# Performance work log

Measured on AMD Instinct MI355X. Metric: run time of the kernel, lower is better.

Reference implementation:

```python
import jax, jax.numpy as jnp
import numpy as np

N = 50000; E = 800000; NFEAT = 128; NHID = 64; CONCAT = 2; NCLASS = 40
D = CONCAT * NHID
BN_EPS = 1e-5


def setup_inputs() -> dict:
    key = jax.random.key(0)
    ks = jax.random.split(key, 16)
    rn = lambda k, s, sc=0.05: jax.random.normal(k, s, jnp.float32) * sc
    return {
        "x1a": rn(ks[0], (N, NFEAT), 1.0),
        "x1b": rn(ks[1], (N, NFEAT), 1.0),
        "x2a": rn(ks[2], (N, NFEAT), 1.0),
        "x2b": rn(ks[3], (N, NFEAT), 1.0),
        "edge_index1": jax.random.randint(ks[4], (2, E), 0, N),
        "edge_index2": jax.random.randint(ks[5], (2, E), 0, N),
        "Wi": rn(ks[6], (CONCAT, NFEAT, NHID)),
        "bi": jnp.zeros((CONCAT, NHID), jnp.float32),
        "gi": jnp.ones((CONCAT, NHID), jnp.float32),
        "bei": jnp.zeros((CONCAT, NHID), jnp.float32),
        "Wm": rn(ks[7], (2, D, D)),
        "bm": jnp.zeros((2, D), jnp.float32),
        "gm": jnp.ones((2, D), jnp.float32),
        "bem": jnp.zeros((2, D), jnp.float32),
        "Wf": rn(ks[8], (D, NCLASS)),
        "bf": jnp.zeros((NCLASS,), jnp.float32),
        "fc1w1_W": rn(ks[9], (D,)),
        "fc1w1_b": jnp.zeros((1,), jnp.float32),
        "fc1w2_W": rn(ks[10], (D,)),
        "fc1w2_b": jnp.zeros((1,), jnp.float32),
        "aws_w1_W": rn(ks[11], (2, D)),
        "aws_w1_b": jnp.zeros((2,), jnp.float32),
        "aws_w2_W": rn(ks[12], (2, D)),
        "aws_w2_b": jnp.zeros((2,), jnp.float32),
        "fcw1_W": rn(ks[13], (NCLASS,)),
        "fcw1_b": jnp.zeros((1,), jnp.float32),
        "fcw2_W": rn(ks[14], (NCLASS,)),
        "fcw2_b": jnp.zeros((1,), jnp.float32),
    }


def _gcn_norm(edge_index, n):
    # GCN symmetric normalization with self-loops (cached=True behaviour)
    loop = jnp.arange(n)
    src = jnp.concatenate([edge_index[0], loop])
    dst = jnp.concatenate([edge_index[1], loop])
    deg = jax.ops.segment_sum(jnp.ones_like(dst, jnp.float32), dst, n)
    dinv = jnp.where(deg > 0, deg ** -0.5, 0.0)
    return src, dst, dinv[src] * dinv[dst]


def _gcn(x, W, b, g):
    # GCNConv: dense projection then sparse scatter-based aggregation
    src, dst, norm = g
    h = x @ W
    agg = jax.ops.segment_sum(h[src] * norm[:, None], dst, x.shape[0])
    return agg + b


def _bn(x, gamma, beta):
    m = x.mean(0)
    v = jnp.mean((x - m) ** 2, axis=0)
    return (x - m) * jax.lax.rsqrt(v + BN_EPS) * gamma + beta


def _gate(x1, x2, w1, b1, w2, b2):
    # sigmoid gates L1-normalized; only the last node's row is used (w[-1,:])
    s1 = jax.nn.sigmoid(jnp.dot(x1[-1], w1) + b1)
    s2 = jax.nn.sigmoid(jnp.dot(x2[-1], w2) + b2)
    t = s1 + s2
    return s1 / t, s2 / t


def _forward(x1a, x1b, x2a, x2b, g1, g2, Wi, bi, gi, bei, Wm, bm, gm, bem,
             Wf, bf, fc1w1_W, fc1w1_b, fc1w2_W, fc1w2_b,
             aws_w1_W, aws_w1_b, aws_w2_W, aws_w2_b,
             fcw1_W, fcw1_b, fcw2_W, fcw2_b):
    xs1, xs2 = (x1a, x1b), (x2a, x2b)
    h1 = jnp.concatenate([jax.nn.relu(_bn(_gcn(xs1[i], Wi[i], bi[i], g1), gi[i], bei[i]))
                          for i in range(CONCAT)], axis=-1)
    h2 = jnp.concatenate([jax.nn.relu(_bn(_gcn(xs2[i], Wi[i], bi[i], g2), gi[i], bei[i]))
                          for i in range(CONCAT)], axis=-1)
    w1, w2 = _gate(h1, h2, fc1w1_W, fc1w1_b[0], fc1w2_W, fc1w2_b[0])
    x = w1 * h1 + w2 * h2
    for i in range(Wm.shape[0]):  # middle layers (n_layers - 2)
        a = jax.nn.relu(_bn(_gcn(x, Wm[i], bm[i], g1), gm[i], bem[i]))
        b = jax.nn.relu(_bn(_gcn(x, Wm[i], bm[i], g2), gm[i], bem[i]))
        w1, w2 = _gate(a, b, aws_w1_W[i], aws_w1_b[i], aws_w2_W[i], aws_w2_b[i])
        x = w1 * a + w2 * b
    p1 = _gcn(x, Wf, bf, g1)
    p2 = _gcn(x, Wf, bf, g2)
    w1, w2 = _gate(p1, p2, fcw1_W, fcw1_b[0], fcw2_W, fcw2_b[0])
    return (w1 * p1 + w2 * p2, p1, p2)


def reference(x1a, x1b, x2a, x2b, edge_index1, edge_index2, Wi, bi, gi, bei,
              Wm, bm, gm, bem, Wf, bf, fc1w1_W, fc1w1_b, fc1w2_W, fc1w2_b,
              aws_w1_W, aws_w1_b, aws_w2_W, aws_w2_b,
              fcw1_W, fcw1_b, fcw2_W, fcw2_b):
    g1 = _gcn_norm(edge_index1, N)
    g2 = _gcn_norm(edge_index2, N)
    return _forward(x1a, x1b, x2a, x2b, g1, g2, Wi, bi, gi, bei, Wm, bm, gm, bem,
                    Wf, bf, fc1w1_W, fc1w1_b, fc1w2_W, fc1w2_b,
                    aws_w1_W, aws_w1_b, aws_w2_W, aws_w2_b,
                    fcw1_W, fcw1_b, fcw2_W, fcw2_b)
```

## Files before the change

kernel.cpp:

```cpp
#include <hip/hip_runtime.h>
#include <hip/hip_fp16.h>


#define DFEAT 128

typedef __attribute__((ext_vector_type(8))) short bf16x8;
typedef __attribute__((ext_vector_type(4))) float f32x4;

__device__ __forceinline__ unsigned short f2bf(float f) {
    unsigned u = __float_as_uint(f);
    u += 0x7fffu + ((u >> 16) & 1u);
    return (unsigned short)(u >> 16);
}
__device__ __forceinline__ float bf2f(unsigned short u) {
    return __uint_as_float((unsigned)u << 16);
}
__device__ __forceinline__ unsigned f2h16(float f) {
    return (unsigned)__half_as_ushort(__float2half(f));
}
__device__ __forceinline__ float h16f(unsigned u) {
    return __half2float(__ushort_as_half((unsigned short)u));
}
__device__ __forceinline__ float4 bf4tof4(ushort4 u) {
    return make_float4(__uint_as_float((unsigned)u.x << 16),
// ... 40 lines not shown
        int s = src[i];
        buf[i - e0] = (d << 16) | s;
        atomicAdd(&cnt8[d >> RSH], 1);
    }
    __syncthreads();
    if (t == 0) {
        int run = 0;
        for (int r = 0; r < nr; ++r) { pre8[r] = run; run += cnt8[r]; }
        pre8[nr] = run;
    }
    __syncthreads();
    if (t < nr) {
        base8[t] = atomicAdd(&gcount[g * NRMAX + t], cnt8[t]);
        cnt8[t] = 0;
    }
    __syncthreads();
    for (int j = t; j < ec; j += 256) {
        int v = buf[j];
        int d = (unsigned)v >> 16;
        int r = d >> RSH;
        int p = pre8[r] + atomicAdd(&cnt8[r], 1);
        buf2[p] = ((d & (RSZ - 1)) << 16) | (v & 0xFFFF);
    }
    __syncthreads();
    for (int j = t; j < ec; j += 256) {
        int r = 0;
        while (j >= pre8[r + 1]) ++r;
        int gpos = base8[r] + (j - pre8[r]);
        if (gpos < SCAP) stg[((size_t)g * NRMAX + r) * SCAP + gpos] = buf2[j];
    }
}

__global__ __launch_bounds__(256) void histB_kernel(
    const int* __restrict__ stg, const int* __restrict__ gcount,
    int* __restrict__ baseB, int nr) {
    int g = blockIdx.y;
    int r = blockIdx.x / SUBS;
    int sub = blockIdx.x % SUBS;
    __shared__ int hist[RSZ];
    int t = threadIdx.x;
    for (int i = t; i < RSZ; i += 256) hist[i] = 0;
    __syncthreads();
    int len = min(gcount[g * NRMAX + r], SCAP);
    int seg = (len + SUBS - 1) / SUBS;
    int e0 = sub * seg, e1 = min(e0 + seg, len);
    const int* sp = stg + ((size_t)g * NRMAX + r) * SCAP;
    for (int i = e0 + t; i < e1; i += 256) atomicAdd(&hist[(unsigned)sp[i] >> 16], 1);
    __syncthreads();
    int* bp = baseB + (((size_t)(g * NRMAX + r) * SUBS + sub) << RSH);
    for (int i = t; i < RSZ; i += 256) bp[i] = hist[i];
}

__global__ __launch_bounds__(256) void scanB_kernel(
    int* __restrict__ baseB, int* __restrict__ cnt1, int* __restrict__ cnt2, int n) {
    int node = blockIdx.x * 256 + threadIdx.x;
    int g = blockIdx.y;
    if (node >= n) return;
    int r = node >> RSH, dloc = node & (RSZ - 1);
    int* p = baseB + (((size_t)(g * NRMAX + r) * SUBS) << RSH) + dloc;
    int run = 0;
#pragma unroll
    for (int s = 0; s < SUBS; ++s) {
        int v = p[(size_t)s << RSH];
        p[(size_t)s << RSH] = run;
        run += v;
    }
    (g ? cnt2 : cnt1)[node] = run;
}

__global__ __launch_bounds__(256) void fillC_kernel(
    const int* __restrict__ stg, const int* __restrict__ gcount,
    const int* __restrict__ baseB,
    const int* __restrict__ rp1, const int* __restrict__ rp2,
    const float* __restrict__ dv1, const float* __restrict__ dv2,
    int* __restrict__ cs1, int* __restrict__ cs2, int n, int nr) {
    int g = blockIdx.y;
    int r = blockIdx.x / SUBS;
    int sub = blockIdx.x % SUBS;
    const int* rp = g ? rp2 : rp1;
    const float* dv = g ? dv2 : dv1;
    int* cs = g ? cs2 : cs1;
    __shared__ int off[RSZ];
    int t = threadIdx.x;
    int r0 = r << RSH;
    int rn = min(RSZ, n - r0);
    if (rn <= 0) return;
    const int* bp = baseB + (((size_t)(g * NRMAX + r) * SUBS + sub) << RSH);
    for (int i = t; i < rn; i += 256) off[i] = bp[i] + rp[r0 + i];
    __syncthreads();
    int len = min(gcount[g * NRMAX + r], SCAP);
    int seg = (len + SUBS - 1) / SUBS;
    int e0 = sub * seg, e1 = min(e0 + seg, len);
    const int* sp = stg + ((size_t)g * NRMAX + r) * SCAP;
    for (int i = e0 + t; i < e1; i += 256) {
        int v = sp[i];
        int dloc = (unsigned)v >> 16;
        int s = v & 0xFFFF;
        float w = dv[r0 + dloc] * dv[s];
        int pos = atomicAdd(&off[dloc], 1);
        cs[pos] = (int)((f2h16(w) << 16) | (unsigned)s);
    }
}

__global__ __launch_bounds__(256) void blocksum_kernel(const int* __restrict__ c1,
                                                       const int* __restrict__ c2,
                                                       int* __restrict__ bs, int n, int nb) {
    const int* c = blockIdx.y ? c2 : c1;
    int* out = bs + (size_t)blockIdx.y * nb;
    int t = threadIdx.x;
    int base = blockIdx.x * 2048 + t * 8;
    int s = 0;
#pragma unroll
    for (int i = 0; i < 8; ++i) {
        int idx = base + i;
        if (idx < n) s += c[idx];
    }
    __shared__ int red[256];
    red[t] = s;
    __syncthreads();
    for (int o = 128; o > 0; o >>= 1) {
        if (t < o) red[t] += red[t + o];
        __syncthreads();
    }
    if (t == 0) out[blockIdx.x] = red[0];
}

__global__ void scansums_kernel(int* __restrict__ bs, int nb, int* __restrict__ rp1,
                                int* __restrict__ rp2, int n, int E, float* __restrict__ stats) {
    int t = threadIdx.x;
    if (t < 2) {
        int* b = bs + (size_t)t * nb;
        int run = 0;
        for (int i = 0; i < nb; ++i) {
            int v = b[i];
            b[i] = run;
            run += v;
        }
        (t ? rp2 : rp1)[n] = E;
    }
    for (int i = t; i < 512; i += 64) stats[i] = 0.f;
}

__global__ __launch_bounds__(256) void writerp_kernel(const int* __restrict__ c1,
                                                      const int* __restrict__ c2,
                                                      const int* __restrict__ bs,
                                                      int* __restrict__ rp1, int* __restrict__ rp2,
                                                      float* __restrict__ dv1,
                                                      float* __restrict__ dv2, int n, int nb) {
    const int* c = blockIdx.y ? c2 : c1;
    int* rp = blockIdx.y ? rp2 : rp1;
    float* dv = blockIdx.y ? dv2 : dv1;
    int boff = bs[(size_t)blockIdx.y * nb + blockIdx.x];
    int t = threadIdx.x;
    int base = blockIdx.x * 2048 + t * 8;
    int v[8];
    int s = 0;
#pragma unroll
    for (int i = 0; i < 8; ++i) {
        int idx = base + i;
        v[i] = (idx < n) ? c[idx] : 0;
        s += v[i];
    }
    __shared__ int red[256];
    red[t] = s;
    __syncthreads();
    for (int o = 1; o < 256; o <<= 1) {
        int x = (t >= o) ? red[t - o] : 0;
        __syncthreads();
        red[t] += x;
        __syncthreads();
    }
    int run = boff + red[t] - s;
#pragma unroll
    for (int i = 0; i < 8; ++i) {
        int idx = base + i;
        if (idx < n) {
            rp[idx] = run;
            dv[idx] = rsqrtf((float)(v[i] + 1));
            run += v[i];
        }
    }
}

template <int COLS, typename OutT>
__global__ __launch_bounds__(256) void dualagg_kernel(
    const unsigned short* __restrict__ h1, const unsigned short* __restrict__ h2,
    const int* __restrict__ rp1, const int* __restrict__ cs1, const float* __restrict__ dv1,
    const int* __restrict__ rp2, const int* __restrict__ cs2, const float* __restrict__ dv2,
    const float* __restrict__ bias, OutT* __restrict__ o1, OutT* __restrict__ o2, int n) {
    constexpr int ACT = COLS / 8;
    const unsigned short* h;
    const int *rp, *cs;
    const float* dv;
    OutT* out;
    if (blockIdx.y == 0) { h = h1; rp = rp1; cs = cs1; dv = dv1; out = o1; }
    else                 { h = h2; rp = rp2; cs = cs2; dv = dv2; out = o2; }
    int wid = blockIdx.x * 4 + (threadIdx.x >> 6);
    if (wid >= n) return;
    int lane = threadIdx.x & 63;
    int grp = lane >> 4;
    int li = lane & 15;
    bool act = li < ACT;
    float acc[8] = {0.f, 0.f, 0.f, 0.f, 0.f, 0.f, 0.f, 0.f};
    int e0 = rp[wid], e1 = rp[wid + 1];
    int e = e0 + grp;
    for (; e + 4 < e1; e += 8) {
        int va = cs[e], vb = cs[e + 4];
        float wa = h16f((unsigned)va >> 16); int sa = va & 0xFFFF;
        float wb = h16f((unsigned)vb >> 16); int sb = vb & 0xFFFF;
        if (act) {
            int4 ra = *(const int4*)(h + (size_t)sa * COLS + li * 8);
            int4 rb = *(const int4*)(h + (size_t)sb * COLS + li * 8);
            acc8(acc, wa, ra);
            acc8(acc, wb, rb);
        }
    }
    if (e < e1) {
        int va = cs[e];
        float wa = h16f((unsigned)va >> 16); int sa = va & 0xFFFF;
        if (act) {
            int4 ra = *(const int4*)(h + (size_t)sa * COLS + li * 8);
            acc8(acc, wa, ra);
        }
    }
#pragma unroll
    for (int j = 0; j < 8; ++j) {
        acc[j] += __shfl_xor(acc[j], 16);
        acc[j] += __shfl_xor(acc[j], 32);
    }
    if (grp == 0 && act) {
        float dn = dv[wid];
        float w = dn * dn;
        int4 rs = *(const int4*)(h + (size_t)wid * COLS + li * 8);
        acc8(acc, w, rs);
        float4 b0 = ((const float4*)bias)[li * 2];
        float4 b1 = ((const float4*)bias)[li * 2 + 1];
        acc[0] += b0.x; acc[1] += b0.y; acc[2] += b0.z; acc[3] += b0.w;
        acc[4] += b1.x; acc[5] += b1.y; acc[6] += b1.z; acc[7] += b1.w;
        if constexpr (sizeof(OutT) == 4) {
            float* op = (float*)out + (size_t)wid * COLS + li * 8;
            *(float4*)op = make_float4(acc[0], acc[1], acc[2], acc[3]);
            *(float4*)(op + 4) = make_float4(acc[4], acc[5], acc[6], acc[7]);
        } else {
            int4 o;
            o.x = (int)((unsigned)f2bf(acc[0]) | ((unsigned)f2bf(acc[1]) << 16));
            o.y = (int)((unsigned)f2bf(acc[2]) | ((unsigned)f2bf(acc[3]) << 16));
            o.z = (int)((unsigned)f2bf(acc[4]) | ((unsigned)f2bf(acc[5]) << 16));
            o.w = (int)((unsigned)f2bf(acc[6]) | ((unsigned)f2bf(acc[7]) << 16));
            *(int4*)((unsigned short*)out + (size_t)wid * COLS + li * 8) = o;
        }
    }
}

__global__ __launch_bounds__(256) void prepW1_kernel(const float* __restrict__ Wi,
                                                     unsigned short* __restrict__ Wt1) {
    int o = blockIdx.x * 256 + threadIdx.x;
    int kk = o & 31;
    int col = (o >> 5) & 63;
    int kc = (o >> 11) & 3;
    int h = (o >> 13) & 1;
    int s = (o >> 14) & 1;
    float w = Wi[(size_t)s * 8192 + (size_t)(kc * 32 + kk) * 64 + col];
    unsigned short hi = f2bf(w);
    Wt1[o] = h ? f2bf(w - bf2f(hi)) : hi;
}

__global__ __launch_bounds__(256) void gemm_l1_kernel(
    const float* __restrict__ x1a, const float* __restrict__ x1b, const float* __restrict__ x2a,
    const float* __restrict__ x2b, const unsigned short* __restrict__ Wt1,
    unsigned short* __restrict__ H1, unsigned short* __restrict__ H2, int nrows) {
    const float* X = (blockIdx.y == 0) ? x1a : (blockIdx.y == 1) ? x1b
                     : (blockIdx.y == 2) ? x2a : x2b;
    int slice = blockIdx.y & 1;
    unsigned short* Y = (blockIdx.y < 2) ? H1 : H2;
    int ocol = slice * 64;
    int tid = threadIdx.x;
    int row0 = blockIdx.x * 64;
    int wave = tid >> 6, lane = tid & 63;
    int m = lane & 15, quad = lane >> 4;
    int arow = row0 + wave * 16 + m;
    bool rv = arow < nrows;
    const float* xp = X + (size_t)arow * DFEAT;
    const unsigned short* Whp = Wt1 + (size_t)slice * 16384;
    const unsigned short* Wlp = Whp + 8192;
    f32x4 acc[4];
#pragma unroll
    for (int i = 0; i < 4; ++i) acc[i] = (f32x4){0.f, 0.f, 0.f, 0.f};
#pragma unroll
    for (int kc = 0; kc < 4; ++kc) {
        float4 f0 = make_float4(0.f, 0.f, 0.f, 0.f);
        float4 f1 = make_float4(0.f, 0.f, 0.f, 0.f);
        if (rv) {
            f0 = *(const float4*)(xp + kc * 32 + quad * 8);
            f1 = *(const float4*)(xp + kc * 32 + quad * 8 + 4);
        }
        float fs[8] = {f0.x, f0.y, f0.z, f0.w, f1.x, f1.y, f1.z, f1.w};
        bf16x8 ah, al;
#pragma unroll
        for (int j = 0; j < 8; ++j) {
            unsigned short hh = f2bf(fs[j]);
            ah[j] = (short)hh;
            al[j] = (short)f2bf(fs[j] - bf2f(hh));
        }
#pragma unroll
        for (int ct = 0; ct < 4; ++ct) {
            int wo = kc * 2048 + (ct * 16 + m) * 32 + quad * 8;
            bf16x8 bh = *(const bf16x8*)(Whp + wo);
            bf16x8 bl = *(const bf16x8*)(Wlp + wo);
            acc[ct] = __builtin_amdgcn_mfma_f32_16x16x32_bf16(ah, bh, acc[ct], 0, 0, 0);
            acc[ct] = __builtin_amdgcn_mfma_f32_16x16x32_bf16(al, bh, acc[ct], 0, 0, 0);
            acc[ct] = __builtin_amdgcn_mfma_f32_16x16x32_bf16(ah, bl, acc[ct], 0, 0, 0);
        }
    }
#pragma unroll
    for (int ct = 0; ct < 4; ++ct) {
#pragma unroll
        for (int i = 0; i < 4; ++i) {
            int gr = row0 + wave * 16 + quad * 4 + i;
            if (gr < nrows) Y[(size_t)gr * DFEAT + ocol + ct * 16 + m] = f2bf(acc[ct][i]);
        }
    }
}

__global__ __launch_bounds__(256) void prepW_kernel(const float* __restrict__ Wm,
                                                    unsigned short* __restrict__ Wt) {
    int o = blockIdx.x * 256 + threadIdx.x;
    int l = blockIdx.y;
    int kk = o & 31;
    int col = (o >> 5) & 127;
    int kc = o >> 12;
    int k = kc * 32 + kk;
    Wt[(size_t)l * 16384 + o] = f2bf(Wm[(size_t)l * 16384 + (size_t)k * 128 + col]);
}

__global__ __launch_bounds__(256) void gemm_mfma_kernel(
    const unsigned short* __restrict__ Abf, const unsigned short* __restrict__ Bbf,
    const float* __restrict__ ss, const float* __restrict__ wout,
    const unsigned short* __restrict__ Wt, unsigned short* __restrict__ Y, int nrows) {
    __shared__ unsigned short Xs[64 * 128];
    int tid = threadIdx.x;
    int row0 = blockIdx.x * 64;
    int wave = tid >> 6, lane = tid & 63;
    int m = lane & 15, quad = lane >> 4;
    float w1 = wout[0], w2 = wout[1];
    for (int u = tid; u < 1024; u += 256) {
        int r = u >> 4;
        int col0 = (u & 15) * 8;
        int gr = row0 + r;
        int swz = (r & 7) << 3;
        if (gr < nrows) {
#pragma unroll
            for (int hh = 0; hh < 2; ++hh) {
                int c = col0 + hh * 4;
                float4 fa = bf4tof4(*(const ushort4*)(Abf + (size_t)gr * 128 + c));
                float4 fb = bf4tof4(*(const ushort4*)(Bbf + (size_t)gr * 128 + c));
                float4 sa = *(const float4*)(ss + c);
                float4 ha = *(const float4*)(ss + 128 + c);
                float4 sb = *(const float4*)(ss + 256 + c);
                float4 hb = *(const float4*)(ss + 384 + c);
                ushort4 o;
                o.x = f2bf(w1 * fmaxf(fmaf(fa.x, sa.x, ha.x), 0.f) +
                           w2 * fmaxf(fmaf(fb.x, sb.x, hb.x), 0.f));
                o.y = f2bf(w1 * fmaxf(fmaf(fa.y, sa.y, ha.y), 0.f) +
                           w2 * fmaxf(fmaf(fb.y, sb.y, hb.y), 0.f));
                o.z = f2bf(w1 * fmaxf(fmaf(fa.z, sa.z, ha.z), 0.f) +
                           w2 * fmaxf(fmaf(fb.z, sb.z, hb.z), 0.f));
                o.w = f2bf(w1 * fmaxf(fmaf(fa.w, sa.w, ha.w), 0.f) +
                           w2 * fmaxf(fmaf(fb.w, sb.w, hb.w), 0.f));
                *(ushort4*)&Xs[r * 128 + (c ^ swz)] = o;
            }
        } else {
            ushort4 z = {0, 0, 0, 0};
            *(ushort4*)&Xs[r * 128 + (col0 ^ swz)] = z;
            *(ushort4*)&Xs[r * 128 + ((col0 + 4) ^ swz)] = z;
        }
    }
    __syncthreads();
    f32x4 acc[8];
#pragma unroll
    for (int i = 0; i < 8; ++i) acc[i] = (f32x4){0.f, 0.f, 0.f, 0.f};
    int arow = wave * 16 + m;
#pragma unroll
    for (int kc = 0; kc < 4; ++kc) {
        int ac = (kc * 32 + quad * 8) ^ ((arow & 7) << 3);
        bf16x8 a = *(const bf16x8*)&Xs[arow * 128 + ac];
// ... 49 lines not shown
            int gr = row0 + r;
            int col0 = kc * 32 + c * 4;
            float4 v = make_float4(0.f, 0.f, 0.f, 0.f);
            if (gr < nrows) {
                float4 a = bf4tof4(*(const ushort4*)(Abf + (size_t)gr * DFEAT + col0));
                float4 b = bf4tof4(*(const ushort4*)(Bbf + (size_t)gr * DFEAT + col0));
                float4 scA = *(const float4*)(ss + col0);
                float4 shA = *(const float4*)(ss + DFEAT + col0);
                float4 scB = *(const float4*)(ss + 2 * DFEAT + col0);
                float4 shB = *(const float4*)(ss + 3 * DFEAT + col0);
                v.x = w1 * fmaxf(fmaf(a.x, scA.x, shA.x), 0.f) +
                      w2 * fmaxf(fmaf(b.x, scB.x, shB.x), 0.f);
                v.y = w1 * fmaxf(fmaf(a.y, scA.y, shA.y), 0.f) +
                      w2 * fmaxf(fmaf(b.y, scB.y, shB.y), 0.f);
                v.z = w1 * fmaxf(fmaf(a.z, scA.z, shA.z), 0.f) +
                      w2 * fmaxf(fmaf(b.z, scB.z, shB.z), 0.f);
                v.w = w1 * fmaxf(fmaf(a.w, scA.w, shA.w), 0.f) +
                      w2 * fmaxf(fmaf(b.w, scB.w, shB.w), 0.f);
            }
            Xs[r][c * 4 + 0] = v.x;
            Xs[r][c * 4 + 1] = v.y;
            Xs[r][c * 4 + 2] = v.z;
            Xs[r][c * 4 + 3] = v.w;
        }
        __syncthreads();
#pragma unroll
        for (int k = 0; k < 32; ++k) {
            float4 w = *(float4*)&Ws[k][cg * 4];
#pragma unroll
            for (int i = 0; i < RPT; ++i) {
                float a = Xs[rg * RPT + i][k];
                acc[i].x = fmaf(a, w.x, acc[i].x);
                acc[i].y = fmaf(a, w.y, acc[i].y);
                acc[i].z = fmaf(a, w.z, acc[i].z);
                acc[i].w = fmaf(a, w.w, acc[i].w);
            }
        }
        __syncthreads();
    }
    if (cg * 4 < fout) {
#pragma unroll
        for (int i = 0; i < RPT; ++i) {
            int r = row0 + rg * RPT + i;
            if (r < nrows) {
                ushort4 o;
                o.x = f2bf(acc[i].x); o.y = f2bf(acc[i].y);
                o.z = f2bf(acc[i].z); o.w = f2bf(acc[i].w);
                *(ushort4*)(Y + (size_t)r * ostride + cg * 4) = o;
            }
        }
    }
}

__global__ __launch_bounds__(256) void stats2_kernel(const unsigned short* __restrict__ A,
                                                     const unsigned short* __restrict__ B,
                                                     float* __restrict__ stats, int nrows) {
    __shared__ float red1[256];
    __shared__ float red2[256];
    int t = threadIdx.x;
    int col = t & 127;
    int rg = t >> 7;
    const unsigned short* src = (blockIdx.y == 0) ? A : B;
    float* st = stats + (size_t)blockIdx.y * 256;
    int r0 = blockIdx.x * 128 + rg * 64;
    int r1 = min(r0 + 64, nrows);
    float s = 0.f, s2 = 0.f;
    for (int r = r0; r < r1; ++r) {
        float v = bf2f(src[(size_t)r * DFEAT + col]);
        s += v;
        s2 = fmaf(v, v, s2);
    }
    red1[t] = s;
    red2[t] = s2;
    __syncthreads();
    if (t < 128) {
        atomicAdd(&st[col], red1[t] + red1[t + 128]);
        atomicAdd(&st[DFEAT + col], red2[t] + red2[t + 128]);
    }
}

__global__ __launch_bounds__(128) void gate_prep_kernel(
    float* __restrict__ statsA, float* __restrict__ statsB,
    const unsigned short* __restrict__ preA, const unsigned short* __restrict__ preB,
    const float* __restrict__ gamma, const float* __restrict__ beta,
    const float* __restrict__ gwA, const float* __restrict__ gbA,
    const float* __restrict__ gwB, const float* __restrict__ gbB,
    float* __restrict__ ss, float* __restrict__ wout, int nrows) {
    __shared__ float red[128];
    __shared__ float dotA_s;
    int t = threadIdx.x;
    float invN = 1.f / (float)nrows;
    float meanA = statsA[t] * invN;
    float varA = statsA[DFEAT + t] * invN - meanA * meanA;
    float scA = gamma[t] * rsqrtf(varA + 1e-5f);
    float shA = beta[t] - meanA * scA;
    ss[t] = scA;
    ss[DFEAT + t] = shA;
    float meanB = statsB[t] * invN;
    float varB = statsB[DFEAT + t] * invN - meanB * meanB;
    float scB = gamma[t] * rsqrtf(varB + 1e-5f);
    float shB = beta[t] - meanB * scB;
    ss[2 * DFEAT + t] = scB;
    ss[3 * DFEAT + t] = shB;
    statsA[t] = 0.f;
    statsA[DFEAT + t] = 0.f;
    statsB[t] = 0.f;
    statsB[DFEAT + t] = 0.f;
    float av = fmaxf(fmaf(bf2f(preA[(size_t)(nrows - 1) * DFEAT + t]), scA, shA), 0.f);
    red[t] = av * gwA[t];
    __syncthreads();
    for (int s = 64; s > 0; s >>= 1) {
        if (t < s) red[t] += red[t + s];
        __syncthreads();
    }
    if (t == 0) dotA_s = red[0];
    __syncthreads();
    float bv = fmaxf(fmaf(bf2f(preB[(size_t)(nrows - 1) * DFEAT + t]), scB, shB), 0.f);
    red[t] = bv * gwB[t];
    __syncthreads();
    for (int s = 64; s > 0; s >>= 1) {
        if (t < s) red[t] += red[t + s];
        __syncthreads();
    }
    if (t == 0) {
        float s1 = 1.f / (1.f + expf(-(dotA_s + gbA[0])));
        float s2 = 1.f / (1.f + expf(-(red[0] + gbB[0])));
        float tt = s1 + s2;
        wout[0] = s1 / tt;
        wout[1] = s2 / tt;
    }
}

__global__ __launch_bounds__(64) void gate_final_kernel(
    const float* __restrict__ p1, const float* __restrict__ p2,
    const float* __restrict__ w1v, const float* __restrict__ b1,
    const float* __restrict__ w2v, const float* __restrict__ b2,
    float* __restrict__ wout, int nrows, int nclass) {
    __shared__ float red[64];
    __shared__ float dot1_s;
    int t = threadIdx.x;
    float v = (t < nclass) ? p1[(size_t)(nrows - 1) * nclass + t] * w1v[t] : 0.f;
    red[t] = v;
    __syncthreads();
    for (int s = 32; s > 0; s >>= 1) {
        if (t < s) red[t] += red[t + s];
        __syncthreads();
    }
    if (t == 0) dot1_s = red[0];
    __syncthreads();
    v = (t < nclass) ? p2[(size_t)(nrows - 1) * nclass + t] * w2v[t] : 0.f;
    red[t] = v;
    __syncthreads();
    for (int s = 32; s > 0; s >>= 1) {
        if (t < s) red[t] += red[t + s];
        __syncthreads();
    }
    if (t == 0) {
        float s1 = 1.f / (1.f + expf(-(dot1_s + b1[0])));
        float s2 = 1.f / (1.f + expf(-(red[0] + b2[0])));
        float tt = s1 + s2;
        wout[0] = s1 / tt;
        wout[1] = s2 / tt;
    }
}

__global__ __launch_bounds__(256) void mix_kernel(const float* __restrict__ p1,
                                                  const float* __restrict__ p2,
                                                  const float* __restrict__ wout,
                                                  float* __restrict__ o, int n4) {
    int idx = blockIdx.x * blockDim.x + threadIdx.x;
    if (idx >= n4) return;
// ... 12 lines not shown
    const int E = in_sizes[4] / 2;
    const int NC = in_sizes[15];

    const float* x1a = (const float*)d_in[0];
    const float* x1b = (const float*)d_in[1];
    const float* x2a = (const float*)d_in[2];
    const float* x2b = (const float*)d_in[3];
    const int* ei1 = (const int*)d_in[4];
    const int* ei2 = (const int*)d_in[5];
    const float* Wi = (const float*)d_in[6];
    const float* bi = (const float*)d_in[7];
    const float* gi = (const float*)d_in[8];
    const float* bei = (const float*)d_in[9];
    const float* Wm = (const float*)d_in[10];
    const float* bm = (const float*)d_in[11];
    const float* gm = (const float*)d_in[12];
    const float* bem = (const float*)d_in[13];
    const float* Wf = (const float*)d_in[14];
    const float* bf = (const float*)d_in[15];
    const float* fc1w1_W = (const float*)d_in[16];
    const float* fc1w1_b = (const float*)d_in[17];
    const float* fc1w2_W = (const float*)d_in[18];
    const float* fc1w2_b = (const float*)d_in[19];
    const float* aws_w1_W = (const float*)d_in[20];
    const float* aws_w1_b = (const float*)d_in[21];
    const float* aws_w2_W = (const float*)d_in[22];
    const float* aws_w2_b = (const float*)d_in[23];
    const float* fcw1_W = (const float*)d_in[24];
    const float* fcw1_b = (const float*)d_in[25];
    const float* fcw2_W = (const float*)d_in[26];
    const float* fcw2_b = (const float*)d_in[27];

    char* ws = (char*)d_ws;
    size_t off = 0;
    auto alloc = [&](size_t bytes) -> char* {
        char* p = ws + off;
        off += (bytes + 255) & ~(size_t)255;
        return p;
    };
    unsigned short* A = (unsigned short*)alloc((size_t)N * DFEAT * 2);
    unsigned short* B = (unsigned short*)alloc((size_t)N * DFEAT * 2);
    unsigned short* H1 = (unsigned short*)alloc((size_t)N * DFEAT * 2);
    unsigned short* H2 = (unsigned short*)alloc((size_t)N * DFEAT * 2);
    int* rp1 = (int*)alloc((size_t)(N + 1) * 4);
    int* rp2 = (int*)alloc((size_t)(N + 1) * 4);
    int* cnt1 = (int*)alloc((size_t)N * 4);
    int* cnt2 = (int*)alloc((size_t)N * 4);
    float* dv1 = (float*)alloc((size_t)N * 4);
    float* dv2 = (float*)alloc((size_t)N * 4);
    int* cs1 = (int*)alloc((size_t)E * 4);
    int* cs2 = (int*)alloc((size_t)E * 4);
    int* stg = (int*)alloc((size_t)2 * NRMAX * SCAP * 4);
    int* baseB = (int*)alloc(((size_t)2 * NRMAX * SUBS << RSH) * 4);
    int* gcount = (int*)alloc(2 * NRMAX * 4);
    unsigned short* Wt = (unsigned short*)alloc((size_t)2 * 16384 * 2);
    unsigned short* Wt1 = (unsigned short*)alloc((size_t)32768 * 2);
    float* stats = (float*)alloc(2048);
    float* statsA = stats;
    float* statsB = stats + 256;
    float* ssbuf = (float*)alloc(2048);
    float* wout = (float*)alloc(256);
    int nb = (N + 2047) / 2048;
    int* bsums = (int*)alloc((size_t)2 * nb * 4);

    const int* src1 = ei1;
    const int* dst1 = ei1 + E;
    const int* src2 = ei2;
    const int* dst2 = ei2 + E;

    int nr = (N + RSZ - 1) >> RSH;
    int gemmbl = (N + 63) / 64;
    dim3 pagrid((E + EPA - 1) / EPA, 2);
    dim3 rsgrid(nr * SUBS, 2);
    dim3 ssgrid((N + 255) / 256, 2);
    dim3 agggrid((N + 3) / 4, 2);
    dim3 statgrid((N + 127) / 128, 2);
    dim3 scangrid(nb, 2);
    dim3 l1grid(gemmbl, 4);
    dim3 prepgrid(64, 2);

    hipMemsetAsync(gcount, 0, 2 * NRMAX * 4, stream);
    prepW_kernel<<<prepgrid, 256, 0, stream>>>(Wm, Wt);
    prepW1_kernel<<<128, 256, 0, stream>>>(Wi, Wt1);
    partA_kernel<<<pagrid, 256, 0, stream>>>(src1, dst1, src2, dst2, stg, gcount, E, nr);
    histB_kernel<<<rsgrid, 256, 0, stream>>>(stg, gcount, baseB, nr);
    scanB_kernel<<<ssgrid, 256, 0, stream>>>(baseB, cnt1, cnt2, N);
    blocksum_kernel<<<scangrid, 256, 0, stream>>>(cnt1, cnt2, bsums, N, nb);
    scansums_kernel<<<1, 64, 0, stream>>>(bsums, nb, rp1, rp2, N, E, stats);
    writerp_kernel<<<scangrid, 256, 0, stream>>>(cnt1, cnt2, bsums, rp1, rp2, dv1, dv2, N, nb);
    fillC_kernel<<<rsgrid, 256, 0, stream>>>(stg, gcount, baseB, rp1, rp2, dv1, dv2,
                                             cs1, cs2, N, nr);

    gemm_l1_kernel<<<l1grid, 256, 0, stream>>>(x1a, x1b, x2a, x2b, Wt1, H1, H2, N);
    dualagg_kernel<128, unsigned short><<<agggrid, 256, 0, stream>>>(
        H1, H2, rp1, cs1, dv1, rp2, cs2, dv2, bi, A, B, N);
    stats2_kernel<<<statgrid, 256, 0, stream>>>(A, B, stats, N);
    gate_prep_kernel<<<1, 128, 0, stream>>>(statsA, statsB, A, B, gi, bei, fc1w1_W, fc1w1_b,
                                            fc1w2_W, fc1w2_b, ssbuf, wout, N);

    gemm_mfma_kernel<<<gemmbl, 256, 0, stream>>>(A, B, ssbuf, wout, Wt, H1, N);
    dualagg_kernel<128, unsigned short><<<agggrid, 256, 0, stream>>>(
        H1, H1, rp1, cs1, dv1, rp2, cs2, dv2, bm, A, B, N);
    stats2_kernel<<<statgrid, 256, 0, stream>>>(A, B, stats, N);
    gate_prep_kernel<<<1, 128, 0, stream>>>(statsA, statsB, A, B, gm, bem, aws_w1_W, aws_w1_b,
                                            aws_w2_W, aws_w2_b, ssbuf, wout, N);

    gemm_mfma_kernel<<<gemmbl, 256, 0, stream>>>(A, B, ssbuf, wout, Wt + 16384, H1, N);
    dualagg_kernel<128, unsigned short><<<agggrid, 256, 0, stream>>>(
        H1, H1, rp1, cs1, dv1, rp2, cs2, dv2, bm + 128, A, B, N);
    stats2_kernel<<<statgrid, 256, 0, stream>>>(A, B, stats, N);
    gate_prep_kernel<<<1, 128, 0, stream>>>(statsA, statsB, A, B, gm + 128, bem + 128,
                                            aws_w1_W + 128, aws_w1_b + 1, aws_w2_W + 128,
                                            aws_w2_b + 1, ssbuf, wout, N);

    float* out0 = (float*)d_out;
    float* p1 = out0 + (size_t)N * NC;
    float* p2 = out0 + (size_t)2 * N * NC;
    gemm_fused_kernel<16, 4><<<gemmbl, 256, 0, stream>>>(A, B, ssbuf, wout, Wf, H2, N, NC, NC);
    dualagg_kernel<40, float><<<agggrid, 256, 0, stream>>>(H2, H2, rp1, cs1, dv1, rp2, cs2, dv2,
                                                           bf, p1, p2, N);
    gate_final_kernel<<<1, 64, 0, stream>>>(p1, p2, fcw1_W, fcw1_b, fcw2_W, fcw2_b, wout, N, NC);
    mix_kernel<<<(N * NC / 4 + 255) / 256, 256, 0, stream>>>(p1, p2, wout, out0, N * NC / 4);
}
```

Baseline: 668.6 us.

## Split 128-col aggregation by column halves and fuse small prep/scan/gate kernels

The 128-wide aggregation kernel is now split across two column halves (grid z), with 8 lanes per edge group and 8 edge groups per wave. The goal is more parallelism and 16 edges in flight per wave. Several small kernels are merged: the two weight-prep kernels and the memset become one prep kernel, the block sums move into scanB, and the BN/gate prep runs in the last block of the stats kernel through an atomic ticket. The gather work per edge is duplicated across the two column halves, and the last-block pattern relies on fences and atomic reads.

Result: slower. 861.5 us (+28.8%).

```diff
diff --git a/kernel.cpp b/kernel.cpp
--- a/kernel.cpp
+++ b/kernel.cpp
@@ -116,20 +116,73 @@
 }
 
 __global__ __launch_bounds__(256) void scanB_kernel(
-    int* __restrict__ baseB, int* __restrict__ cnt1, int* __restrict__ cnt2, int n) {
+    int* __restrict__ baseB, int* __restrict__ cnt1, int* __restrict__ cnt2,
+    int* __restrict__ bsums, int n, int nb) {
     int node = blockIdx.x * 256 + threadIdx.x;
     int g = blockIdx.y;
-    if (node >= n) return;
-    int r = node >> RSH, dloc = node & (RSZ - 1);
-    int* p = baseB + (((size_t)(g * NRMAX + r) * SUBS) << RSH) + dloc;
+    int t = threadIdx.x;
     int run = 0;
-#pragma unroll
-    for (int s = 0; s < SUBS; ++s) {
-        int v = p[(size_t)s << RSH];
-        p[(size_t)s << RSH] = run;
-        run += v;
-    }
-    (g ? cnt2 : cnt1)[node] = run;
+    if (node < n) {
+        int r = node >> RSH, dloc = node & (RSZ - 1);
+        int* p = baseB + (((size_t)(g * NRMAX + r) * SUBS) << RSH) + dloc;
+#pragma unroll
+        for (int s = 0; s < SUBS; ++s) {
+            int v = p[(size_t)s << RSH];
+            p[(size_t)s << RSH] = run;
+            run += v;
+        }
+        (g ? cnt2 : cnt1)[node] = run;
+    }
+    __shared__ int red[256];
+    red[t] = run;
+    __syncthreads();
+    for (int o = 128; o > 0; o >>= 1) {
+        if (t < o) red[t] += red[t + o];
+        __syncthreads();
+    }
+    if (t == 0) bsums[(size_t)g * nb + blockIdx.x] = red[0];
+}
+
+__global__ void scansums_kernel(int* __restrict__ bs, int nb, int* __restrict__ rp1,
+                                int* __restrict__ rp2, int n, int E, float* __restrict__ stats) {
+    int t = threadIdx.x;
+    if (t < 2) {
+        int* b = bs + (size_t)t * nb;
+        int run = 0;
+        for (int i = 0; i < nb; ++i) {
+            int v = b[i];
+            b[i] = run;
+            run += v;
+        }
+        (t ? rp2 : rp1)[n] = E;
+    }
+    for (int i = t; i < 512; i += 64) stats[i] = 0.f;
+}
+
+__global__ __launch_bounds__(256) void writerp_kernel(
+    const int* __restrict__ c1, const int* __restrict__ c2, const int* __restrict__ bs,
+    int* __restrict__ rp1, int* __restrict__ rp2,
+    float* __restrict__ dv1, float* __restrict__ dv2, int n, int nb) {
+    const int* c = blockIdx.y ? c2 : c1;
+    int* rp = blockIdx.y ? rp2 : rp1;
+    float* dv = blockIdx.y ? dv2 : dv1;
+    int t = threadIdx.x;
+    int node = blockIdx.x * 256 + t;
+    int v = (node < n) ? c[node] : 0;
+    __shared__ int red[256];
+    red[t] = v;
+    __syncthreads();
+    for (int o = 1; o < 256; o <<= 1) {
+        int x = (t >= o) ? red[t - o] : 0;
+        __syncthreads();
+        red[t] += x;
+        __syncthreads();
+    }
+    if (node < n) {
+        int run = bs[(size_t)blockIdx.y * nb + blockIdx.x] + red[t] - v;
+        rp[node] = run;
+        dv[node] = rsqrtf((float)(v + 1));
+    }
 }
 
 __global__ __launch_bounds__(256) void fillC_kernel(
@@ -166,97 +219,77 @@
     }
 }
 
-__global__ __launch_bounds__(256) void blocksum_kernel(const int* __restrict__ c1,
-                                                       const int* __restrict__ c2,
-                                                       int* __restrict__ bs, int n, int nb) {
-    const int* c = blockIdx.y ? c2 : c1;
-    int* out = bs + (size_t)blockIdx.y * nb;
-    int t = threadIdx.x;
-    int base = blockIdx.x * 2048 + t * 8;
-    int s = 0;
-#pragma unroll
-    for (int i = 0; i < 8; ++i) {
-        int idx = base + i;
-        if (idx < n) s += c[idx];
-    }
-    __shared__ int red[256];
-    red[t] = s;
-    __syncthreads();
-    for (int o = 128; o > 0; o >>= 1) {
-        if (t < o) red[t] += red[t + o];
-        __syncthreads();
-    }
-    if (t == 0) out[blockIdx.x] = red[0];
-}
-
-__global__ void scansums_kernel(int* __restrict__ bs, int nb, int* __restrict__ rp1,
-                                int* __restrict__ rp2, int n, int E, float* __restrict__ stats) {
-    int t = threadIdx.x;
-    if (t < 2) {
-        int* b = bs + (size_t)t * nb;
-        int run = 0;
-        for (int i = 0; i < nb; ++i) {
-            int v = b[i];
-            b[i] = run;
-            run += v;
-        }
-        (t ? rp2 : rp1)[n] = E;
-    }
-    for (int i = t; i < 512; i += 64) stats[i] = 0.f;
-}
-
-__global__ __launch_bounds__(256) void writerp_kernel(const int* __restrict__ c1,
-                                                      const int* __restrict__ c2,
-                                                      const int* __restrict__ bs,
-                                                      int* __restrict__ rp1, int* __restrict__ rp2,
-                                                      float* __restrict__ dv1,
-                                                      float* __restrict__ dv2, int n, int nb) {
-    const int* c = blockIdx.y ? c2 : c1;
-    int* rp = blockIdx.y ? rp2 : rp1;
-    float* dv = blockIdx.y ? dv2 : dv1;
-    int boff = bs[(size_t)blockIdx.y * nb + blockIdx.x];
-    int t = threadIdx.x;
-    int base = blockIdx.x * 2048 + t * 8;
-    int v[8];
-    int s = 0;
-#pragma unroll
-    for (int i = 0; i < 8; ++i) {
-        int idx = base + i;
-        v[i] = (idx < n) ? c[idx] : 0;
-        s += v[i];
-    }
-    __shared__ int red[256];
-    red[t] = s;
-    __syncthreads();
-    for (int o = 1; o < 256; o <<= 1) {
-        int x = (t >= o) ? red[t - o] : 0;
-        __syncthreads();
-        red[t] += x;
-        __syncthreads();
-    }
-    int run = boff + red[t] - s;
-#pragma unroll
-    for (int i = 0; i < 8; ++i) {
-        int idx = base + i;
-        if (idx < n) {
-            rp[idx] = run;
-            dv[idx] = rsqrtf((float)(v[i] + 1));
-            run += v[i];
-        }
-    }
-}
-
-template <int COLS, typename OutT>
-__global__ __launch_bounds__(256) void dualagg_kernel(
+__global__ __launch_bounds__(256) void dualagg128_kernel(
     const unsigned short* __restrict__ h1, const unsigned short* __restrict__ h2,
     const int* __restrict__ rp1, const int* __restrict__ cs1, const float* __restrict__ dv1,
     const int* __restrict__ rp2, const int* __restrict__ cs2, const float* __restrict__ dv2,
-    const float* __restrict__ bias, OutT* __restrict__ o1, OutT* __restrict__ o2, int n) {
+    const float* __restrict__ bias, unsigned short* __restrict__ o1,
+    unsigned short* __restrict__ o2, int n) {
+    const unsigned short* h;
+    const int *rp, *cs;
+    const float* dv;
+    unsigned short* out;
+    if (blockIdx.y == 0) { h = h1; rp = rp1; cs = cs1; dv = dv1; out = o1; }
+    else                 { h = h2; rp = rp2; cs = cs2; dv = dv2; out = o2; }
+    int wid = blockIdx.x * 4 + (threadIdx.x >> 6);
+    if (wid >= n) return;
+    int lane = threadIdx.x & 63;
+    int grp = lane >> 3;
+    int li = lane & 7;
+    int colbase = (int)blockIdx.z * 64 + li * 8;
+    float acc[8] = {0.f, 0.f, 0.f, 0.f, 0.f, 0.f, 0.f, 0.f};
+    int e0 = rp[wid], e1 = rp[wid + 1];
+    int e = e0 + grp;
+    for (; e + 8 < e1; e += 16) {
+        int va = cs[e], vb = cs[e + 8];
+        float wa = h16f((unsigned)va >> 16); int sa = va & 0xFFFF;
+        float wb = h16f((unsigned)vb >> 16); int sb = vb & 0xFFFF;
+        int4 ra = *(const int4*)(h + (size_t)sa * 128 + colbase);
+        int4 rb = *(const int4*)(h + (size_t)sb * 128 + colbase);
+        acc8(acc, wa, ra);
+        acc8(acc, wb, rb);
+    }
+    if (e < e1) {
+        int va = cs[e];
+        float wa = h16f((unsigned)va >> 16); int sa = va & 0xFFFF;
+        int4 ra = *(const int4*)(h + (size_t)sa * 128 + colbase);
+        acc8(acc, wa, ra);
+    }
+#pragma unroll
+    for (int j = 0; j < 8; ++j) {
+        acc[j] += __shfl_xor(acc[j], 8);
+        acc[j] += __shfl_xor(acc[j], 16);
+        acc[j] += __shfl_xor(acc[j], 32);
+    }
+    if (grp == 0) {
+        float dn = dv[wid];
+        float w = dn * dn;
+        int4 rs = *(const int4*)(h + (size_t)wid * 128 + colbase);
+        acc8(acc, w, rs);
+        float4 b0 = *(const float4*)(bias + colbase);
+        float4 b1 = *(const float4*)(bias + colbase + 4);
+        acc[0] += b0.x; acc[1] += b0.y; acc[2] += b0.z; acc[3] += b0.w;
+        acc[4] += b1.x; acc[5] += b1.y; acc[6] += b1.z; acc[7] += b1.w;
+        int4 o;
+        o.x = (int)((unsigned)f2bf(acc[0]) | ((unsigned)f2bf(acc[1]) << 16));
+        o.y = (int)((unsigned)f2bf(acc[2]) | ((unsigned)f2bf(acc[3]) << 16));
+        o.z = (int)((unsigned)f2bf(acc[4]) | ((unsigned)f2bf(acc[5]) << 16));
+        o.w = (int)((unsigned)f2bf(acc[6]) | ((unsigned)f2bf(acc[7]) << 16));
+        *(int4*)(out + (size_t)wid * 128 + colbase) = o;
+    }
+}
+
+__global__ __launch_bounds__(256) void dualagg_final_kernel(
+    const unsigned short* __restrict__ h1, const unsigned short* __restrict__ h2,
+    const int* __restrict__ rp1, const int* __restrict__ cs1, const float* __restrict__ dv1,
+    const int* __restrict__ rp2, const int* __restrict__ cs2, const float* __restrict__ dv2,
+    const float* __restrict__ bias, float* __restrict__ o1, float* __restrict__ o2, int n) {
+    constexpr int COLS = 40;
     constexpr int ACT = COLS / 8;
     const unsigned short* h;
     const int *rp, *cs;
     const float* dv;
-    OutT* out;
+    float* out;
     if (blockIdx.y == 0) { h = h1; rp = rp1; cs = cs1; dv = dv1; out = o1; }
     else                 { h = h2; rp = rp2; cs = cs2; dv = dv2; out = o2; }
     int wid = blockIdx.x * 4 + (threadIdx.x >> 6);
@@ -301,32 +334,40 @@
         float4 b1 = ((const float4*)bias)[li * 2 + 1];
         acc[0] += b0.x; acc[1] += b0.y; acc[2] += b0.z; acc[3] += b0.w;
         acc[4] += b1.x; acc[5] += b1.y; acc[6] += b1.z; acc[7] += b1.w;
-        if constexpr (sizeof(OutT) == 4) {
-            float* op = (float*)out + (size_t)wid * COLS + li * 8;
-            *(float4*)op = make_float4(acc[0], acc[1], acc[2], acc[3]);
-            *(float4*)(op + 4) = make_float4(acc[4], acc[5], acc[6], acc[7]);
-        } else {
-            int4 o;
-            o.x = (int)((unsigned)f2bf(acc[0]) | ((unsigned)f2bf(acc[1]) << 16));
-            o.y = (int)((unsigned)f2bf(acc[2]) | ((unsigned)f2bf(acc[3]) << 16));
-            o.z = (int)((unsigned)f2bf(acc[4]) | ((unsigned)f2bf(acc[5]) << 16));
-            o.w = (int)((unsigned)f2bf(acc[6]) | ((unsigned)f2bf(acc[7]) << 16));
-            *(int4*)((unsigned short*)out + (size_t)wid * COLS + li * 8) = o;
-        }
-    }
-}
-
-__global__ __launch_bounds__(256) void prepW1_kernel(const float* __restrict__ Wi,
-                                                     unsigned short* __restrict__ Wt1) {
-    int o = blockIdx.x * 256 + threadIdx.x;
-    int kk = o & 31;
-    int col = (o >> 5) & 63;
-    int kc = (o >> 11) & 3;
-    int h = (o >> 13) & 1;
-    int s = (o >> 14) & 1;
-    float w = Wi[(size_t)s * 8192 + (size_t)(kc * 32 + kk) * 64 + col];
-    unsigned short hi = f2bf(w);
-    Wt1[o] = h ? f2bf(w - bf2f(hi)) : hi;
+        float* op = out + (size_t)wid * COLS + li * 8;
+        *(float4*)op = make_float4(acc[0], acc[1], acc[2], acc[3]);
+        *(float4*)(op + 4) = make_float4(acc[4], acc[5], acc[6], acc[7]);
+    }
+}
+
+__global__ __launch_bounds__(256) void prep_kernel(const float* __restrict__ Wm,
+                                                   const float* __restrict__ Wi,
+                                                   unsigned short* __restrict__ Wt,
+                                                   unsigned short* __restrict__ Wt1,
+                                                   int* __restrict__ zeros) {
+    int b = blockIdx.x;
+    int t = threadIdx.x;
+    if (b < 128) {
+        int l = b >> 6;
+        int o = (b & 63) * 256 + t;
+        int kk = o & 31;
+        int col = (o >> 5) & 127;
+        int kc = o >> 12;
+        int k = kc * 32 + kk;
+        Wt[(size_t)l * 16384 + o] = f2bf(Wm[(size_t)l * 16384 + (size_t)k * 128 + col]);
+    } else if (b < 256) {
+        int o = (b - 128) * 256 + t;
+        int kk = o & 31;
+        int col = (o >> 5) & 63;
+        int kc = (o >> 11) & 3;
+        int hsel = (o >> 13) & 1;
+        int s = (o >> 14) & 1;
+        float w = Wi[(size_t)s * 8192 + (size_t)(kc * 32 + kk) * 64 + col];
+        unsigned short hi = f2bf(w);
+        Wt1[o] = hsel ? f2bf(w - bf2f(hi)) : hi;
+    } else {
+        if (t < 32) zeros[t] = 0;
+    }
 }
 
 __global__ __launch_bounds__(256) void gemm_l1_kernel(
@@ -384,17 +425,6 @@
             if (gr < nrows) Y[(size_t)gr * DFEAT + ocol + ct * 16 + m] = f2bf(acc[ct][i]);
         }
     }
-}
-
-__global__ __launch_bounds__(256) void prepW_kernel(const float* __restrict__ Wm,
-                                                    unsigned short* __restrict__ Wt) {
-    int o = blockIdx.x * 256 + threadIdx.x;
-    int l = blockIdx.y;
-    int kk = o & 31;
-    int col = (o >> 5) & 127;
-    int kc = o >> 12;
-    int k = kc * 32 + kk;
-    Wt[(size_t)l * 16384 + o] = f2bf(Wm[(size_t)l * 16384 + (size_t)k * 128 + col]);
 }
 
 __global__ __launch_bounds__(256) void gemm_mfma_kernel(
@@ -550,62 +580,74 @@
     }
 }
 
-__global__ __launch_bounds__(256) void stats2_kernel(const unsigned short* __restrict__ A,
-                                                     const unsigned short* __restrict__ B,
-                                                     float* __restrict__ stats, int nrows) {
+__global__ __launch_bounds__(256) void stats2g_kernel(
+    const unsigned short* __restrict__ A, const unsigned short* __restrict__ B,
+    float* __restrict__ stats, int nrows,
+    const float* __restrict__ gamma, const float* __restrict__ beta,
+    const float* __restrict__ gwA, const float* __restrict__ gbA,
+    const float* __restrict__ gwB, const float* __restrict__ gbB,
+    float* __restrict__ ss, float* __restrict__ wout, unsigned* __restrict__ tick) {
     __shared__ float red1[256];
     __shared__ float red2[256];
     int t = threadIdx.x;
-    int col = t & 127;
-    int rg = t >> 7;
-    const unsigned short* src = (blockIdx.y == 0) ? A : B;
-    float* st = stats + (size_t)blockIdx.y * 256;
-    int r0 = blockIdx.x * 128 + rg * 64;
-    int r1 = min(r0 + 64, nrows);
-    float s = 0.f, s2 = 0.f;
-    for (int r = r0; r < r1; ++r) {
-        float v = bf2f(src[(size_t)r * DFEAT + col]);
-        s += v;
-        s2 = fmaf(v, v, s2);
-    }
-    red1[t] = s;
-    red2[t] = s2;
-    __syncthreads();
-    if (t < 128) {
-        atomicAdd(&st[col], red1[t] + red1[t + 128]);
-        atomicAdd(&st[DFEAT + col], red2[t] + red2[t + 128]);
-    }
-}
-
-__global__ __launch_bounds__(128) void gate_prep_kernel(
-    float* __restrict__ statsA, float* __restrict__ statsB,
-    const unsigned short* __restrict__ preA, const unsigned short* __restrict__ preB,
-    const float* __restrict__ gamma, const float* __restrict__ beta,
-    const float* __restrict__ gwA, const float* __restrict__ gbA,
-    const float* __restrict__ gwB, const float* __restrict__ gbB,
-    float* __restrict__ ss, float* __restrict__ wout, int nrows) {
+    {
+        int col = t & 127;
+        int rg = t >> 7;
+        const unsigned short* src = (blockIdx.y == 0) ? A : B;
+        float* st = stats + (size_t)blockIdx.y * 256;
+        int r0 = blockIdx.x * 128 + rg * 64;
+        int r1 = min(r0 + 64, nrows);
+        float s = 0.f, s2 = 0.f;
+        for (int r = r0; r < r1; ++r) {
+            float v = bf2f(src[(size_t)r * DFEAT + col]);
+            s += v;
+            s2 = fmaf(v, v, s2);
+        }
+        red1[t] = s;
+        red2[t] = s2;
+        __syncthreads();
+        if (t < 128) {
+            atomicAdd(&st[col], red1[t] + red1[t + 128]);
+            atomicAdd(&st[DFEAT + col], red2[t] + red2[t + 128]);
+        }
+    }
+    __threadfence();
+    __shared__ int amlast;
+    __syncthreads();
+    if (t == 0) {
+        unsigned v = atomicAdd(tick, 1u);
+        amlast = (v == gridDim.x * gridDim.y - 1) ? 1 : 0;
+    }
+    __syncthreads();
+    if (!amlast) return;
     __shared__ float red[128];
     __shared__ float dotA_s;
-    int t = threadIdx.x;
     float invN = 1.f / (float)nrows;
-    float meanA = statsA[t] * invN;
-    float varA = statsA[DFEAT + t] * invN - meanA * meanA;
-    float scA = gamma[t] * rsqrtf(varA + 1e-5f);
-    float shA = beta[t] - meanA * scA;
-    ss[t] = scA;
-    ss[DFEAT + t] = shA;
-    float meanB = statsB[t] * invN;
-    float varB = statsB[DFEAT + t] * invN - meanB * meanB;
-    float scB = gamma[t] * rsqrtf(varB + 1e-5f);
-    float shB = beta[t] - meanB * scB;
-    ss[2 * DFEAT + t] = scB;
-    ss[3 * DFEAT + t] = shB;
-    statsA[t] = 0.f;
-    statsA[DFEAT + t] = 0.f;
-    statsB[t] = 0.f;
-    statsB[DFEAT + t] = 0.f;
-    float av = fmaxf(fmaf(bf2f(preA[(size_t)(nrows - 1) * DFEAT + t]), scA, shA), 0.f);
-    red[t] = av * gwA[t];
+    float scA = 0.f, shA = 0.f, scB = 0.f, shB = 0.f;
+    if (t < 128) {
+        float sA = atomicAdd(&stats[t], 0.f);
+        float s2A = atomicAdd(&stats[DFEAT + t], 0.f);
+        float sB = atomicAdd(&stats[256 + t], 0.f);
+        float s2B = atomicAdd(&stats[256 + DFEAT + t], 0.f);
+        float meanA = sA * invN;
+        float varA = s2A * invN - meanA * meanA;
+        scA = gamma[t] * rsqrtf(varA + 1e-5f);
+        shA = beta[t] - meanA * scA;
+        ss[t] = scA;
+        ss[DFEAT + t] = shA;
+        float meanB = sB * invN;
+        float varB = s2B * invN - meanB * meanB;
+        scB = gamma[t] * rsqrtf(varB + 1e-5f);
+        shB = beta[t] - meanB * scB;
+        ss[2 * DFEAT + t] = scB;
+        ss[3 * DFEAT + t] = shB;
+        stats[t] = 0.f;
+        stats[DFEAT + t] = 0.f;
+        stats[256 + t] = 0.f;
+        stats[256 + DFEAT + t] = 0.f;
+        float av = fmaxf(fmaf(bf2f(A[(size_t)(nrows - 1) * DFEAT + t]), scA, shA), 0.f);
+        red[t] = av * gwA[t];
+    }
     __syncthreads();
     for (int s = 64; s > 0; s >>= 1) {
         if (t < s) red[t] += red[t + s];
@@ -613,8 +655,10 @@
     }
     if (t == 0) dotA_s = red[0];
     __syncthreads();
-    float bv = fmaxf(fmaf(bf2f(preB[(size_t)(nrows - 1) * DFEAT + t]), scB, shB), 0.f);
-    red[t] = bv * gwB[t];
+    if (t < 128) {
+        float bv = fmaxf(fmaf(bf2f(B[(size_t)(nrows - 1) * DFEAT + t]), scB, shB), 0.f);
+        red[t] = bv * gwB[t];
+    }
     __syncthreads();
     for (int s = 64; s > 0; s >>= 1) {
         if (t < s) red[t] += red[t + s];
@@ -733,15 +777,14 @@
     int* cs2 = (int*)alloc((size_t)E * 4);
     int* stg = (int*)alloc((size_t)2 * NRMAX * SCAP * 4);
     int* baseB = (int*)alloc(((size_t)2 * NRMAX * SUBS << RSH) * 4);
-    int* gcount = (int*)alloc(2 * NRMAX * 4);
+    int* gcount = (int*)alloc(32 * 4);
+    unsigned* tick = (unsigned*)(gcount + 24);
     unsigned short* Wt = (unsigned short*)alloc((size_t)2 * 16384 * 2);
     unsigned short* Wt1 = (unsigned short*)alloc((size_t)32768 * 2);
     float* stats = (float*)alloc(2048);
-    float* statsA = stats;
-    float* statsB = stats + 256;
     float* ssbuf = (float*)alloc(2048);
     float* wout = (float*)alloc(256);
-    int nb = (N + 2047) / 2048;
+    int nb = (N + 255) / 256;
     int* bsums = (int*)alloc((size_t)2 * nb * 4);
 
     const int* src1 = ei1;
@@ -753,53 +796,46 @@
     int gemmbl = (N + 63) / 64;
     dim3 pagrid((E + EPA - 1) / EPA, 2);
     dim3 rsgrid(nr * SUBS, 2);
-    dim3 ssgrid((N + 255) / 256, 2);
-    dim3 agggrid((N + 3) / 4, 2);
+    dim3 nodegrid(nb, 2);
+    dim3 agggrid((N + 3) / 4, 2, 2);
+    dim3 aggfgrid((N + 3) / 4, 2);
     dim3 statgrid((N + 127) / 128, 2);
-    dim3 scangrid(nb, 2);
     dim3 l1grid(gemmbl, 4);
-    dim3 prepgrid(64, 2);
-
-    hipMemsetAsync(gcount, 0, 2 * NRMAX * 4, stream);
-    prepW_kernel<<<prepgrid, 256, 0, stream>>>(Wm, Wt);
-    prepW1_kernel<<<128, 256, 0, stream>>>(Wi, Wt1);
+
+    prep_kernel<<<257, 256, 0, stream>>>(Wm, Wi, Wt, Wt1, gcount);
     partA_kernel<<<pagrid, 256, 0, stream>>>(src1, dst1, src2, dst2, stg, gcount, E, nr);
     histB_kernel<<<rsgrid, 256, 0, stream>>>(stg, gcount, baseB, nr);
-    scanB_kernel<<<ssgrid, 256, 0, stream>>>(baseB, cnt1, cnt2, N);
-    blocksum_kernel<<<scangrid, 256, 0, stream>>>(cnt1, cnt2, bsums, N, nb);
+    scanB_kernel<<<nodegrid, 256, 0, stream>>>(baseB, cnt1, cnt2, bsums, N, nb);
     scansums_kernel<<<1, 64, 0, stream>>>(bsums, nb, rp1, rp2, N, E, stats);
-    writerp_kernel<<<scangrid, 256, 0, stream>>>(cnt1, cnt2, bsums, rp1, rp2, dv1, dv2, N, nb);
+    writerp_kernel<<<nodegrid, 256, 0, stream>>>(cnt1, cnt2, bsums, rp1, rp2, dv1, dv2, N, nb);
     fillC_kernel<<<rsgrid, 256, 0, stream>>>(stg, gcount, baseB, rp1, rp2, dv1, dv2,
                                              cs1, cs2, N, nr);
 
     gemm_l1_kernel<<<l1grid, 256, 0, stream>>>(x1a, x1b, x2a, x2b, Wt1, H1, H2, N);
-    dualagg_kernel<128, unsigned short><<<agggrid, 256, 0, stream>>>(
-        H1, H2, rp1, cs1, dv1, rp2, cs2, dv2, bi, A, B, N);
-    stats2_kernel<<<statgrid, 256, 0, stream>>>(A, B, stats, N);
-    gate_prep_kernel<<<1, 128, 0, stream>>>(statsA, statsB, A, B, gi, bei, fc1w1_W, fc1w1_b,
-                                            fc1w2_W, fc1w2_b, ssbuf, wout, N);
+    dualagg128_kernel<<<agggrid, 256, 0, stream>>>(H1, H2, rp1, cs1, dv1, rp2, cs2, dv2,
+                                                   bi, A, B, N);
+    stats2g_kernel<<<statgrid, 256, 0, stream>>>(A, B, stats, N, gi, bei, fc1w1_W, fc1w1_b,
+                                                 fc1w2_W, fc1w2_b, ssbuf, wout, tick);
 
     gemm_mfma_kernel<<<gemmbl, 256, 0, stream>>>(A, B, ssbuf, wout, Wt, H1, N);
-    dualagg_kernel<128, unsigned short><<<agggrid, 256, 0, stream>>>(
-        H1, H1, rp1, cs1, dv1, rp2, cs2, dv2, bm, A, B, N);
-    stats2_kernel<<<statgrid, 256, 0, stream>>>(A, B, stats, N);
-    gate_prep_kernel<<<1, 128, 0, stream>>>(statsA, statsB, A, B, gm, bem, aws_w1_W, aws_w1_b,
-                                            aws_w2_W, aws_w2_b, ssbuf, wout, N);
+    dualagg128_kernel<<<agggrid, 256, 0, stream>>>(H1, H1, rp1, cs1, dv1, rp2, cs2, dv2,
+                                                   bm, A, B, N);
+    stats2g_kernel<<<statgrid, 256, 0, stream>>>(A, B, stats, N, gm, bem, aws_w1_W, aws_w1_b,
+                                                 aws_w2_W, aws_w2_b, ssbuf, wout, tick + 1);
 
     gemm_mfma_kernel<<<gemmbl, 256, 0, stream>>>(A, B, ssbuf, wout, Wt + 16384, H1, N);
-    dualagg_kernel<128, unsigned short><<<agggrid, 256, 0, stream>>>(
-        H1, H1, rp1, cs1, dv1, rp2, cs2, dv2, bm + 128, A, B, N);
-    stats2_kernel<<<statgrid, 256, 0, stream>>>(A, B, stats, N);
-    gate_prep_kernel<<<1, 128, 0, stream>>>(statsA, statsB, A, B, gm + 128, bem + 128,
-                                            aws_w1_W + 128, aws_w1_b + 1, aws_w2_W + 128,
-                                            aws_w2_b + 1, ssbuf, wout, N);
+    dualagg128_kernel<<<agggrid, 256, 0, stream>>>(H1, H1, rp1, cs1, dv1, rp2, cs2, dv2,
+                                                   bm + 128, A, B, N);
+    stats2g_kernel<<<statgrid, 256, 0, stream>>>(A, B, stats, N, gm + 128, bem + 128,
+                                                 aws_w1_W + 128, aws_w1_b + 1, aws_w2_W + 128,
+                                                 aws_w2_b + 1, ssbuf, wout, tick + 2);
 
     float* out0 = (float*)d_out;
     float* p1 = out0 + (size_t)N * NC;
     float* p2 = out0 + (size_t)2 * N * NC;
     gemm_fused_kernel<16, 4><<<gemmbl, 256, 0, stream>>>(A, B, ssbuf, wout, Wf, H2, N, NC, NC);
-    dualagg_kernel<40, float><<<agggrid, 256, 0, stream>>>(H2, H2, rp1, cs1, dv1, rp2, cs2, dv2,
-                                                           bf, p1, p2, N);
+    dualagg_final_kernel<<<aggfgrid, 256, 0, stream>>>(H2, H2, rp1, cs1, dv1, rp2, cs2, dv2,
+                                                       bf, p1, p2, N);
     gate_final_kernel<<<1, 64, 0, stream>>>(p1, p2, fcw1_W, fcw1_b, fcw2_W, fcw2_b, wout, N, NC);
     mix_kernel<<<(N * NC / 4 + 255) / 256, 256, 0, stream>>>(p1, p2, wout, out0, N * NC / 4);
 }
```
